# Performance work log

Hardware: AMD Instinct MI355X
Metric: run time of the kernel (lower is better)

Reference implementation:

```python
import jax, jax.numpy as jnp
import numpy as np

MIN_LEN_SEG = 19
MAX_LEN_SEG = 32
MIN_LEN_SEQ = 64
MAX_LEN_SEQ = 128
MAX_LEN_PAD = 192
MAX_NUM_SEG = MAX_LEN_SEQ // MIN_LEN_SEG + 1   # 7
SEG_GRID = 2 * MAX_LEN_SEG                      # 64 candidate positions per segment
B = 4096
C = 80


def setup_inputs() -> dict:
    key = jax.random.key(0)
    k1, k2, k3, k4 = jax.random.split(key, 4)
    x = jax.random.normal(k1, (B, MAX_LEN_PAD, C), dtype=jnp.float32)
    # valid lengths in [min_len_seq, max_len_seq] so warped seq fits in max_len_pad
    len_seq = jax.random.randint(k2, (B,), MIN_LEN_SEQ, MAX_LEN_SEQ + 1, dtype=jnp.int32)
    # raw uniforms; +0.5 applied inside reference (scale in [0.5, 1.5))
    scales = jax.random.uniform(k3, (B * MAX_NUM_SEG,), dtype=jnp.float32)
    # raw segment lengths; +MIN_LEN_SEG applied inside (len_seg in [19, 32))
    len_seg_raw = jax.random.randint(k4, (B * MAX_NUM_SEG,), 0,
                                     MAX_LEN_SEG - MIN_LEN_SEG, dtype=jnp.int32)
    return {"x": x, "len_seq": len_seq, "scales": scales, "len_seg_raw": len_seg_raw}


def reference(x, len_seq, scales, len_seg_raw):
    """Random segment-wise time warp with linear interpolation.
    x: (B, T=MAX_LEN_PAD, C). Returns (B, MAX_LEN_PAD, C), each row's warped
    sequence left-aligned and zero-padded (matching the original pad+stack)."""
    Bsz, T, Cdim = x.shape
    N = Bsz * MAX_NUM_SEG

    scale = scales + 0.5                                   # (N,) in [0.5, 1.5)
    idx = jnp.arange(SEG_GRID, dtype=jnp.float32)          # (L,)
    idx_scaled = idx[None, :] / scale[:, None]             # (N, L)
    idx_fl = jnp.floor(idx_scaled)
    lam = idx_scaled - idx_fl                              # (N, L) interp weight

    len_seg = len_seg_raw + MIN_LEN_SEG                    # (N,) in [19, 32)
    mask_seg = idx_fl < (len_seg[:, None].astype(jnp.float32) - 1.0)

    # cumulative segment offsets within each batch element
    offset = jnp.cumsum(len_seg.reshape(Bsz, MAX_NUM_SEG), axis=-1)
    offset = jnp.pad(offset[:, :-1], ((0, 0), (1, 0))).reshape(N, 1)  # (N,1)
    idx_org = idx_fl + offset.astype(jnp.float32)          # (N, L) source frame

    len_seq_rp = jnp.repeat(len_seq, MAX_NUM_SEG)          # (N,)
    mask_org = idx_org < (len_seq_rp[:, None] - 1).astype(jnp.float32)
    mask = mask_seg & mask_org                             # (N, L)

    # gather floor/ceil frames from the input
    idx_org_i = jnp.clip(idx_org.astype(jnp.int32), 0, T - 2)  # safe when masked
    bidx = jnp.repeat(jnp.arange(Bsz), MAX_NUM_SEG)        # (N,)
    y_fl = x[bidx[:, None], idx_org_i]                     # (N, L, C)
    y_cl = x[bidx[:, None], idx_org_i + 1]                 # (N, L, C)
    y = (1.0 - lam[..., None]) * y_fl + lam[..., None] * y_cl

    # left-pack valid positions per batch element via cumsum, scatter into output
    mask_b = mask.reshape(Bsz, MAX_NUM_SEG * SEG_GRID)     # (B, S*L)
    pos = jnp.cumsum(mask_b.astype(jnp.int32), axis=-1) - 1
    # invalid or overflowing entries go to dump slot MAX_LEN_PAD
    pos = jnp.where(mask_b & (pos < MAX_LEN_PAD), pos, MAX_LEN_PAD)
    y_b = jnp.where(mask_b[..., None], y.reshape(Bsz, MAX_NUM_SEG * SEG_GRID, Cdim), 0.0)

    out = jnp.zeros((Bsz, MAX_LEN_PAD + 1, Cdim), dtype=x.dtype)
    out = out.at[jnp.arange(Bsz)[:, None], pos].add(y_b)
    return out[:, :MAX_LEN_PAD]
```

## Files before the change

kernel.cpp:

```cpp
#include <hip/hip_runtime.h>

#define MIN_LEN_SEG_C 19
#define MAX_NUM_SEG_C 7
#define SEG_GRID_C    64
#define MAX_LEN_PAD_C 192
#define C_DIM         80
#define NQ            (C_DIM / 4)
#define NTHREADS      448
#define TOTAL_Q       (MAX_LEN_PAD_C * NQ)
#define NITER         ((TOTAL_Q + NTHREADS - 1) / NTHREADS)

typedef float floatx4 __attribute__((ext_vector_type(4)));

__global__ __launch_bounds__(NTHREADS) void interp_lnr_kernel(
    const float* __restrict__ x,
    const int*   __restrict__ len_seq,
    const float* __restrict__ scales,
    const int*   __restrict__ len_seg_raw,
    float*       __restrict__ out)
{
    const int b    = blockIdx.x;
    const int tid  = threadIdx.x;
    const int wave = tid >> 6;
    const int lane = tid & 63;

    __shared__ float s_scale[MAX_NUM_SEG_C];
    __shared__ int   s_lenseg[MAX_NUM_SEG_C];
    __shared__ int   s_wavecnt[MAX_NUM_SEG_C];
    __shared__ int   s_src[MAX_LEN_PAD_C];
    __shared__ float s_lam[MAX_LEN_PAD_C];

    if (tid < MAX_NUM_SEG_C) {
        s_scale[tid]  = scales[b * MAX_NUM_SEG_C + tid] + 0.5f;
        s_lenseg[tid] = len_seg_raw[b * MAX_NUM_SEG_C + tid] + MIN_LEN_SEG_C;
    }
    if (tid < MAX_LEN_PAD_C) {
        s_src[tid] = -1;
    }
    __syncthreads();

    const int lseq = len_seq[b];

    const float scale = s_scale[wave];
    int offset = 0;
    for (int t = 0; t < wave; ++t) offset += s_lenseg[t];

    const float idx_scaled = (float)lane / scale;
    const float idx_fl     = floorf(idx_scaled);
    const float lam        = idx_scaled - idx_fl;
    const float idx_org    = idx_fl + (float)offset;

    const bool mask = (idx_fl  < (float)s_lenseg[wave] - 1.0f) &&
                      (idx_org < (float)(lseq - 1));

    const unsigned long long bal = __ballot(mask);
    if (lane == 0) s_wavecnt[wave] = __popcll(bal);
    __syncthreads();

    int wave_off = 0;
    for (int t = 0; t < wave; ++t) wave_off += s_wavecnt[t];
    const int rank = __popcll(bal & ((1ull << lane) - 1ull));

    if (mask) {
        const int pos = wave_off + rank;
        if (pos < MAX_LEN_PAD_C) {
            int src = (int)idx_org;
            src = min(src, MAX_LEN_PAD_C - 2);
            s_src[pos] = src;
            s_lam[pos] = lam;
        }
    }
    __syncthreads();

    const floatx4* __restrict__ x4 =
        (const floatx4*)(x + (size_t)b * MAX_LEN_PAD_C * C_DIM);
    floatx4* __restrict__ out4 =
        (floatx4*)(out + (size_t)b * MAX_LEN_PAD_C * C_DIM);

    int   srcs[NITER];
    float lams[NITER];
    int   qs[NITER];

    #pragma unroll
    for (int i = 0; i < NITER; ++i) {
        const int t = tid + i * NTHREADS;
        if (t < TOTAL_Q) {
            const int p = t / NQ;
            qs[i]   = t - p * NQ;
            srcs[i] = s_src[p];
            lams[i] = s_lam[p];
        } else {
            srcs[i] = -2;
            qs[i]   = 0;
            lams[i] = 0.0f;
        }
    }

    floatx4 va[NITER], vc[NITER];
    #pragma unroll
    for (int i = 0; i < NITER; ++i) {
        if (srcs[i] >= 0) {
            const int base = srcs[i] * NQ + qs[i];
            va[i] = x4[base];
            vc[i] = x4[base + NQ];
        }
    }

    #pragma unroll
    for (int i = 0; i < NITER; ++i) {
        const int t = tid + i * NTHREADS;
        if (srcs[i] >= -1) {
            floatx4 r = (floatx4)(0.0f);
            if (srcs[i] >= 0) {
                const float lm = lams[i];
                const float w0 = 1.0f - lm;
                r = w0 * va[i] + lm * vc[i];
            }
            __builtin_nontemporal_store(r, &out4[t]);
        }
    }
}

extern "C" void kernel_launch(void* const* d_in, const int* in_sizes, int n_in,
                              void* d_out, int out_size, void* d_ws, size_t ws_size,
                              hipStream_t stream) {
    const float* x           = (const float*)d_in[0];
    const int*   len_seq     = (const int*)d_in[1];
    const float* scales      = (const float*)d_in[2];
    const int*   len_seg_raw = (const int*)d_in[3];
    float*       out         = (float*)d_out;

    const int B = in_sizes[1];

    interp_lnr_kernel<<<B, NTHREADS, 0, stream>>>(x, len_seq, scales, len_seg_raw, out);
}
```

Measured before the change: 393.7 us.

## Stage valid input rows into LDS with async global_load_lds before interpolation

Each block now copies the first len_seq rows of its input slice into shared memory with asynchronous global-to-LDS loads. This copy overlaps with the mask, prefix and offset computation. The interpolation then reads its floor and ceil frames from LDS rather than issuing duplicated global gathers. Segment parameters are read straight into registers instead of through shared memory. The cost is about 43 KB of LDS per block, which lowers occupancy, and the code depends on the barrier correctly waiting for the async LDS loads to finish.

Measured after the change: 402.9 us. 1.02x slower.

```diff
diff --git a/kernel.cpp b/kernel.cpp
--- a/kernel.cpp
+++ b/kernel.cpp
@@ -2,13 +2,16 @@
 
 #define MIN_LEN_SEG_C 19
 #define MAX_NUM_SEG_C 7
-#define SEG_GRID_C    64
 #define MAX_LEN_PAD_C 192
 #define C_DIM         80
 #define NQ            (C_DIM / 4)
 #define NTHREADS      448
 #define TOTAL_Q       (MAX_LEN_PAD_C * NQ)
 #define NITER         ((TOTAL_Q + NTHREADS - 1) / NTHREADS)
+#define ROW_BYTES     (C_DIM * 4)
+#define BLOCK_CHUNK   (NTHREADS * 16)
+#define MAX_ROUNDS    6
+#define SX_FLOATS     (MAX_ROUNDS * BLOCK_CHUNK / 4)
 
 typedef float floatx4 __attribute__((ext_vector_type(4)));
 
@@ -24,97 +27,85 @@
     const int wave = tid >> 6;
     const int lane = tid & 63;
 
-    __shared__ float s_scale[MAX_NUM_SEG_C];
-    __shared__ int   s_lenseg[MAX_NUM_SEG_C];
-    __shared__ int   s_wavecnt[MAX_NUM_SEG_C];
+    __shared__ float s_x[SX_FLOATS];
     __shared__ int   s_src[MAX_LEN_PAD_C];
     __shared__ float s_lam[MAX_LEN_PAD_C];
-
-    if (tid < MAX_NUM_SEG_C) {
-        s_scale[tid]  = scales[b * MAX_NUM_SEG_C + tid] + 0.5f;
-        s_lenseg[tid] = len_seg_raw[b * MAX_NUM_SEG_C + tid] + MIN_LEN_SEG_C;
-    }
-    if (tid < MAX_LEN_PAD_C) {
-        s_src[tid] = -1;
-    }
-    __syncthreads();
+    __shared__ int   s_wavecnt[MAX_NUM_SEG_C];
 
     const int lseq = len_seq[b];
 
-    const float scale = s_scale[wave];
+    {
+        const char* gx = (const char*)(x + (size_t)b * MAX_LEN_PAD_C * C_DIM);
+        char*       lx = (char*)s_x;
+        const int rounds = (lseq * ROW_BYTES + BLOCK_CHUNK - 1) / BLOCK_CHUNK;
+        for (int r = 0; r < rounds; ++r) {
+            const int chunk = r * BLOCK_CHUNK + wave * 1024;
+            __builtin_amdgcn_global_load_lds(
+                (const __attribute__((address_space(1))) void*)(gx + chunk + lane * 16),
+                (__attribute__((address_space(3))) void*)(lx + chunk),
+                16, 0, 0);
+        }
+    }
+
+    int lensegs[MAX_NUM_SEG_C];
+    #pragma unroll
+    for (int t = 0; t < MAX_NUM_SEG_C; ++t)
+        lensegs[t] = len_seg_raw[b * MAX_NUM_SEG_C + t] + MIN_LEN_SEG_C;
+    const float scale = scales[b * MAX_NUM_SEG_C + wave] + 0.5f;
+
     int offset = 0;
-    for (int t = 0; t < wave; ++t) offset += s_lenseg[t];
+    int lenw   = lensegs[0];
+    #pragma unroll
+    for (int t = 1; t < MAX_NUM_SEG_C; ++t) {
+        if (wave >= t) offset += lensegs[t - 1];
+        if (wave == t) lenw    = lensegs[t];
+    }
 
     const float idx_scaled = (float)lane / scale;
     const float idx_fl     = floorf(idx_scaled);
     const float lam        = idx_scaled - idx_fl;
     const float idx_org    = idx_fl + (float)offset;
 
-    const bool mask = (idx_fl  < (float)s_lenseg[wave] - 1.0f) &&
+    const bool mask = (idx_fl  < (float)lenw - 1.0f) &&
                       (idx_org < (float)(lseq - 1));
 
     const unsigned long long bal = __ballot(mask);
     if (lane == 0) s_wavecnt[wave] = __popcll(bal);
+    if (tid < MAX_LEN_PAD_C) s_src[tid] = -1;
     __syncthreads();
 
     int wave_off = 0;
-    for (int t = 0; t < wave; ++t) wave_off += s_wavecnt[t];
+    #pragma unroll
+    for (int t = 0; t < MAX_NUM_SEG_C - 1; ++t)
+        if (wave > t) wave_off += s_wavecnt[t];
     const int rank = __popcll(bal & ((1ull << lane) - 1ull));
 
     if (mask) {
         const int pos = wave_off + rank;
         if (pos < MAX_LEN_PAD_C) {
-            int src = (int)idx_org;
-            src = min(src, MAX_LEN_PAD_C - 2);
-            s_src[pos] = src;
+            s_src[pos] = (int)idx_org;
             s_lam[pos] = lam;
         }
     }
     __syncthreads();
 
-    const floatx4* __restrict__ x4 =
-        (const floatx4*)(x + (size_t)b * MAX_LEN_PAD_C * C_DIM);
     floatx4* __restrict__ out4 =
         (floatx4*)(out + (size_t)b * MAX_LEN_PAD_C * C_DIM);
-
-    int   srcs[NITER];
-    float lams[NITER];
-    int   qs[NITER];
+    const floatx4* s_x4 = (const floatx4*)s_x;
 
     #pragma unroll
     for (int i = 0; i < NITER; ++i) {
         const int t = tid + i * NTHREADS;
         if (t < TOTAL_Q) {
             const int p = t / NQ;
-            qs[i]   = t - p * NQ;
-            srcs[i] = s_src[p];
-            lams[i] = s_lam[p];
-        } else {
-            srcs[i] = -2;
-            qs[i]   = 0;
-            lams[i] = 0.0f;
-        }
-    }
-
-    floatx4 va[NITER], vc[NITER];
-    #pragma unroll
-    for (int i = 0; i < NITER; ++i) {
-        if (srcs[i] >= 0) {
-            const int base = srcs[i] * NQ + qs[i];
-            va[i] = x4[base];
-            vc[i] = x4[base + NQ];
-        }
-    }
-
-    #pragma unroll
-    for (int i = 0; i < NITER; ++i) {
-        const int t = tid + i * NTHREADS;
-        if (srcs[i] >= -1) {
+            const int q = t - p * NQ;
+            const int src = s_src[p];
             floatx4 r = (floatx4)(0.0f);
-            if (srcs[i] >= 0) {
-                const float lm = lams[i];
-                const float w0 = 1.0f - lm;
-                r = w0 * va[i] + lm * vc[i];
+            if (src >= 0) {
+                const float lm = s_lam[p];
+                const floatx4 va = s_x4[src * NQ + q];
+                const floatx4 vc = s_x4[src * NQ + q + NQ];
+                r = (1.0f - lm) * va + lm * vc;
             }
             __builtin_nontemporal_store(r, &out4[t]);
         }
```
